# Kernel optimization log

Hardware: AMD Instinct MI355X
Metric: run time of the kernel (lower is better)

The kernel has to match this reference:

```python
import jax, jax.numpy as jnp
import numpy as np

B, T, D = 256, 261, 768      # batch, tokens (1 cls + 4 reg + 16*16 patches), embed_dim
NUM_REG = 4
G = 16                       # patch grid side = 224 // 14
ROI = 3                      # roi_side


def setup_inputs() -> dict:
    key = jax.random.key(0)
    k1, k2 = jax.random.split(key)
    tokens = jax.random.normal(k1, (B, T, D), jnp.float32)
    W_proj = jax.random.normal(k2, (D, D), jnp.float32) * (1.0 / np.sqrt(D))
    b_proj = jnp.zeros((D,), jnp.float32)
    return {"tokens": tokens, "W_proj": W_proj, "b_proj": b_proj}


def _buddy_pool_all(cues, patches2d):
    # cues: [B, C, d]; patches2d: [B, H, W, d]
    Bn, H, W, d = patches2d.shape
    flat = patches2d.reshape(Bn, H * W, d)
    sim = jnp.einsum('bcd,bnd->bcn', cues, flat)          # [B, C, HW]
    idx = jnp.argmax(sim, axis=-1)                         # [B, C]
    h, w = idx // W, idx % W
    r = ROI // 2
    rows = jnp.arange(H)
    cols = jnp.arange(W)
    # clipped ROI window == torch slice(max(0,h-r), min(H,h+r+1)) as a mask
    rmask = (rows[None, None, :] >= (h - r)[..., None]) & (rows[None, None, :] <= (h + r)[..., None])  # [B,C,H]
    cmask = (cols[None, None, :] >= (w - r)[..., None]) & (cols[None, None, :] <= (w + r)[..., None])  # [B,C,W]
    mask = (rmask[..., :, None] & cmask[..., None, :]).astype(patches2d.dtype)  # [B,C,H,W]
    roi_sum = jnp.einsum('bchw,bhwd->bcd', mask, patches2d)
    cnt = jnp.sum(mask, axis=(-2, -1))[..., None]          # 4, 6, or 9 at borders
    return roi_sum / cnt                                   # [B, C, d]


def reference(tokens, W_proj, b_proj):
    t = tokens @ W_proj.T + b_proj                         # nn.Linear projection
    cues = t[:, : 1 + NUM_REG, :]                          # cls + registers: [B,5,d]
    patches2d = t[:, 1 + NUM_REG :, :].reshape(t.shape[0], G, G, D)
    rois = _buddy_pool_all(cues, patches2d)                # [B,5,d]
    toks = jnp.concatenate([cues, rois], axis=1)           # [B,10,d]
    n = jnp.linalg.norm(toks, axis=-1, keepdims=True)
    return toks / jnp.maximum(n, 1e-12)                    # F.normalize
```

## Files before the change

### kernel.cpp

```cpp
#include <hip/hip_runtime.h>
#include <math.h>

constexpr int kB = 256;
constexpr int kT = 261;
constexpr int kD = 768;
constexpr int kC = 5;
constexpr int kG = 16;
constexpr int kP = 256;
constexpr int kTok = kT * kD;
constexpr float kTau = 0.03f;
constexpr int kSlots = 64;

typedef short short8v __attribute__((ext_vector_type(8)));
typedef float f32x4 __attribute__((ext_vector_type(4)));
typedef unsigned short ushort_t;

__device__ inline ushort_t f2bf(float x) {
    unsigned int u = __float_as_uint(x);
    unsigned int r = (u + 0x7FFFu + ((u >> 16) & 1u)) >> 16;
    return (ushort_t)r;
}
__device__ inline float bf2f(ushort_t h) { return __uint_as_float(((unsigned int)h) << 16); }


__global__ __launch_bounds__(256)
void kprep(const float* __restrict__ W,
           ushort_t* __restrict__ Wb_hi, ushort_t* __restrict__ Wb_lo,
           ushort_t* __restrict__ Wt_hi, ushort_t* __restrict__ Wt_lo)
{
    __shared__ ushort_t Lhi[32][36], Llo[32][36];
    const int blk = blockIdx.x, tr = blk / 24, tc = blk % 24;
    const int t = threadIdx.x, r = t >> 3, q = t & 7;
    const int row = tr * 32 + r, col = tc * 32 + q * 4;
    const float4 v = *(const float4*)&W[(size_t)row * kD + col];
    const ushort_t h0 = f2bf(v.x), h1 = f2bf(v.y), h2 = f2bf(v.z), h3 = f2bf(v.w);
    const ushort_t l0 = f2bf(v.x - bf2f(h0)), l1 = f2bf(v.y - bf2f(h1));
    const ushort_t l2 = f2bf(v.z - bf2f(h2)), l3 = f2bf(v.w - bf2f(h3));
    *(ushort4*)&Wb_hi[(size_t)row * kD + col] = make_ushort4(h0, h1, h2, h3);
    *(ushort4*)&Wb_lo[(size_t)row * kD + col] = make_ushort4(l0, l1, l2, l3);
    Lhi[r][q*4+0] = h0; Lhi[r][q*4+1] = h1; Lhi[r][q*4+2] = h2; Lhi[r][q*4+3] = h3;
    Llo[r][q*4+0] = l0; Llo[r][q*4+1] = l1; Llo[r][q*4+2] = l2; Llo[r][q*4+3] = l3;
    __syncthreads();
    const size_t orow = (size_t)(tc * 32 + r) * kD + tr * 32 + q * 4;
    *(ushort4*)&Wt_hi[orow] = make_ushort4(Lhi[q*4+0][r], Lhi[q*4+1][r], Lhi[q*4+2][r], Lhi[q*4+3][r]);
    *(ushort4*)&Wt_lo[orow] = make_ushort4(Llo[q*4+0][r], Llo[q*4+1][r], Llo[q*4+2][r], Llo[q*4+3][r]);
}

template<int MODE>
__global__ __launch_bounds__(256)
void kmm(const float* __restrict__ tokens,
         const ushort_t* __restrict__ Bhi, const ushort_t* __restrict__ Blo,
         const float* __restrict__ bvec, const float* __restrict__ Asrc,
         float* __restrict__ dstA, float* __restrict__ dstB)
{
    __shared__ ushort_t Ah[32][40], Al[32][40];
    __shared__ ushort_t Bh[32][40], Bl[32][40];
    const int mt = blockIdx.x, nt = blockIdx.y, t = threadIdx.x;
    const int w = t >> 6, l = t & 63;
    const int ln = l & 15, kq = l >> 4;
    const int mf = w & 1, nf = w >> 1;
    const int ar = t >> 3, aq = t & 7;
    const int br = t >> 3, bq = t & 7;

    const int am = mt * 32 + ar;
    const float* __restrict__ Ap = (MODE == 0) ? tokens : Asrc;
    const size_t arow = (MODE == 0)
        ? ((size_t)(am / 5) * kTok + (size_t)(am % 5) * kD)
        : ((size_t)am * kD);
    const size_t brow = (size_t)(nt * 32 + br) * kD;

    float4 pa; ushort4 pbh, pbl;
    auto load_regs = [&](int kc) {
        pa  = *(const float4*)&Ap[arow + kc + aq * 4];
        pbh = *(const ushort4*)&Bhi[brow + kc + bq * 4];
        pbl = *(const ushort4*)&Blo[brow + kc + bq * 4];
    };
    auto write_lds = [&]() {
        const ushort_t h0 = f2bf(pa.x), h1 = f2bf(pa.y), h2 = f2bf(pa.z), h3 = f2bf(pa.w);
        const ushort_t a0 = f2bf(pa.x - bf2f(h0)), a1 = f2bf(pa.y - bf2f(h1));
        const ushort_t a2 = f2bf(pa.z - bf2f(h2)), a3 = f2bf(pa.w - bf2f(h3));
        *(ushort4*)&Ah[ar][aq * 4] = make_ushort4(h0, h1, h2, h3);
        *(ushort4*)&Al[ar][aq * 4] = make_ushort4(a0, a1, a2, a3);
        *(ushort4*)&Bh[br][bq * 4] = pbh;
        *(ushort4*)&Bl[br][bq * 4] = pbl;
    };

    f32x4 acc = {0.f, 0.f, 0.f, 0.f};
    auto compute = [&]() {
        const short8v ah  = *(const short8v*)&Ah[mf * 16 + ln][kq * 8];
        const short8v al_ = *(const short8v*)&Al[mf * 16 + ln][kq * 8];
        const short8v bh  = *(const short8v*)&Bh[nf * 16 + ln][kq * 8];
        const short8v bl  = *(const short8v*)&Bl[nf * 16 + ln][kq * 8];
        acc = __builtin_amdgcn_mfma_f32_16x16x32_bf16(al_, bh, acc, 0, 0, 0);
        acc = __builtin_amdgcn_mfma_f32_16x16x32_bf16(ah,  bl, acc, 0, 0, 0);
        acc = __builtin_amdgcn_mfma_f32_16x16x32_bf16(ah,  bh, acc, 0, 0, 0);
    };

    load_regs(0);
    write_lds();
    __syncthreads();
    for (int kc = 32; kc < kD; kc += 32) {
        load_regs(kc);
        compute();
        __syncthreads();
        write_lds();
        __syncthreads();
    }
    compute();

    const int col = nt * 32 + nf * 16 + ln;
    const float bb = (MODE != 1) ? bvec[col] : 0.f;
    #pragma unroll
    for (int r = 0; r < 4; ++r) {
        const int row = mt * 32 + mf * 16 + kq * 4 + r;
        const float val = acc[r] + bb;
        if (MODE == 0) {
            dstA[(size_t)row * kD + col] = val;
            dstB[((size_t)(row / 5) * 10 + (row % 5)) * kD + col] = val;
        } else if (MODE == 1) {
            dstA[(size_t)row * kD + col] = val;
        } else {
            dstA[((size_t)(row / 5) * 10 + 5 + (row % 5)) * kD + col] = val;
        }
    }
}

__global__ __launch_bounds__(256)
void ksim(const float* __restrict__ tokens, const float* __restrict__ u_all,
          float* __restrict__ simsp)
{
    __shared__ ushort_t Uh[6][392], Ul[6][392];
    const int b = blockIdx.x, pq = blockIdx.y, kh = blockIdx.z;
    const int t = threadIdx.x;
    const int w = t >> 6, lane = t & 63;
    const int ln = lane & 15, kq = lane >> 4;
    const size_t tb = (size_t)b * kTok;

    for (int i = t; i < 384; i += 256) {
        const int gd = kh * 384 + i;
        #pragma unroll
        for (int c = 0; c < kC; ++c) {
            const float v = u_all[(size_t)b * kC * kD + (size_t)c * kD + gd];
            const ushort_t h = f2bf(v);
            Uh[c][i] = h; Ul[c][i] = f2bf(v - bf2f(h));
        }
        Uh[kC][i] = 0; Ul[kC][i] = 0;
    }
    __syncthreads();

    const int urow = (ln < kC) ? ln : kC;
    const int n0 = pq * 64 + w * 16;
    const float* __restrict__ prow =
        &tokens[tb + (size_t)(kC + n0 + ln) * kD + kh * 384 + kq * 8];

    f32x4 acc = {0.f, 0.f, 0.f, 0.f};
    #pragma unroll
    for (int c = 0; c < 12; ++c) {
        const float4 fa = *(const float4*)&prow[c * 32];
        const float4 fb = *(const float4*)&prow[c * 32 + 4];
        const float fv[8] = {fa.x, fa.y, fa.z, fa.w, fb.x, fb.y, fb.z, fb.w};
        short8v bh, bl;
        #pragma unroll
        for (int j = 0; j < 8; ++j) {
            const ushort_t h = f2bf(fv[j]);
            bh[j] = (short)h;
            bl[j] = (short)f2bf(fv[j] - bf2f(h));
        }
        const short8v ah  = *(const short8v*)&Uh[urow][c * 32 + kq * 8];
        const short8v al_ = *(const short8v*)&Ul[urow][c * 32 + kq * 8];
        acc = __builtin_amdgcn_mfma_f32_16x16x32_bf16(al_, bh, acc, 0, 0, 0);
        acc = __builtin_amdgcn_mfma_f32_16x16x32_bf16(ah,  bl, acc, 0, 0, 0);
        acc = __builtin_amdgcn_mfma_f32_16x16x32_bf16(ah,  bh, acc, 0, 0, 0);
    }
    float* __restrict__ sp = simsp + (size_t)kh * (1280 * (size_t)kP);
    const int n = n0 + ln;
    if (kq == 0) {
        #pragma unroll
        for (int r = 0; r < 4; ++r)
            sp[((size_t)b * kC + r) * kP + n] = acc[r];
    } else if (kq == 1) {
        sp[((size_t)b * kC + 4) * kP + n] = acc[0];
    }
}

__global__ __launch_bounds__(64)
void ktop(const float* __restrict__ simsp, int* __restrict__ bestn,
          int* __restrict__ cnt, int* __restrict__ flist)
{
    const int pair = blockIdx.x;
    const int lane = threadIdx.x;
    const float* s0 = &simsp[(size_t)pair * kP];
    const float* s1 = &simsp[1280 * (size_t)kP + (size_t)pair * kP];
    float m1 = -3.4e38f, m2 = -3.4e38f; int i1 = 0;
    #pragma unroll
    for (int k = 0; k < 4; ++k) {
        const int n = lane + k * 64;
        const float v = s0[n] + s1[n];
        if (v > m1 || (v == m1 && n < i1)) { m2 = m1; m1 = v; i1 = n; }
        else if (v > m2) m2 = v;
    }
    #pragma unroll
    for (int off = 32; off >= 1; off >>= 1) {
        const float om1 = __shfl_xor(m1, off, 64);
        const int   oi1 = __shfl_xor(i1, off, 64);
        const float om2 = __shfl_xor(m2, off, 64);
        float nm2 = fmaxf(m2, om2);
        if (om1 > m1 || (om1 == m1 && oi1 < i1)) { nm2 = fmaxf(nm2, m1); m1 = om1; i1 = oi1; }
        else nm2 = fmaxf(nm2, om1);
        m2 = nm2;
    }
    if (lane == 0) {
        bestn[pair] = i1;
        if (m1 - m2 < kTau) {
            const int i = atomicAdd(cnt, 1);
            if (i < kSlots) flist[i] = pair;
        }
    }
}

__global__ __launch_bounds__(256)
void kr_tcb(const float* __restrict__ tokens, const float* __restrict__ W,
            const float* __restrict__ bvec, const int* __restrict__ cnt,
            const int* __restrict__ flist, double* __restrict__ tcb64g)
{
    const int slot = blockIdx.x;
    if (slot >= min(*cnt, kSlots)) return;
    const int pair = flist[slot];
    const int b = pair / 5, c = pair % 5;
    const int js = blockIdx.y;
    const int t = threadIdx.x, w = t >> 6, lane = t & 63;
    const size_t tb = (size_t)b * kTok;

    const float* cuep = &tokens[tb + (size_t)c * kD + lane * 4];
    const float4 cf0 = *(const float4*)&cuep[0];
    const float4 cf1 = *(const float4*)&cuep[256];
    const float4 cf2 = *(const float4*)&cuep[512];
    for (int it = 0; it < 16; ++it) {
        const int j = js * 64 + it * 4 + w;
        const float* wr = &W[(size_t)j * kD + lane * 4];
        const float4 w0 = *(const float4*)&wr[0];
        const float4 w1 = *(const float4*)&wr[256];
        const float4 w2 = *(const float4*)&wr[512];
        double acc = (double)w0.x*cf0.x + (double)w0.y*cf0.y + (double)w0.z*cf0.z + (double)w0.w*cf0.w
                   + (double)w1.x*cf1.x + (double)w1.y*cf1.y + (double)w1.z*cf1.z + (double)w1.w*cf1.w
                   + (double)w2.x*cf2.x + (double)w2.y*cf2.y + (double)w2.z*cf2.z + (double)w2.w*cf2.w;
        #pragma unroll
        for (int off = 32; off >= 1; off >>= 1)
            acc += __shfl_xor(acc, off, 64);
        if (lane == 0) tcb64g[(size_t)slot * kD + j] = acc + (double)bvec[j];
    }
}

__global__ __launch_bounds__(256)
void kr_u(const float* __restrict__ W, const int* __restrict__ cnt,
          const double* __restrict__ tcb64g, double* __restrict__ u64g)
{
    const int slot = blockIdx.x;
    if (slot >= min(*cnt, kSlots)) return;
    __shared__ double part[4][64];
    const int t = threadIdx.x;
    const int i = t & 63, jq = t >> 6;
    const int i0 = blockIdx.y * 64;

    const double* tc = &tcb64g[(size_t)slot * kD + jq * 192];
    const float* wp = &W[(size_t)(jq * 192) * kD + i0 + i];
    double acc = 0.0;
    #pragma unroll 8
    for (int j = 0; j < 192; ++j)
        acc += tc[j] * (double)wp[(size_t)j * kD];
    part[jq][i] = acc;
    __syncthreads();
    if (t < 64)
        u64g[(size_t)slot * kD + i0 + t] = part[0][t] + part[1][t] + part[2][t] + part[3][t];
}

__global__ __launch_bounds__(256)
void kr_sim(const float* __restrict__ tokens, const int* __restrict__ cnt,
            const int* __restrict__ flist, const double* __restrict__ u64g,
            double* __restrict__ s64g)
{
    const int slot = blockIdx.x;
    if (slot >= min(*cnt, kSlots)) return;
    __shared__ double u64s[kD];
    const int pair = flist[slot];
    const int b = pair / 5;
    const int ps = blockIdx.y;
    const int t = threadIdx.x, w = t >> 6, lane = t & 63;
    const size_t tb = (size_t)b * kTok;

    u64s[t]       = u64g[(size_t)slot * kD + t];
    u64s[t + 256] = u64g[(size_t)slot * kD + t + 256];
    u64s[t + 512] = u64g[(size_t)slot * kD + t + 512];
    __syncthreads();

    #pragma unroll
    for (int it = 0; it < 8; ++it) {
        const int n = ps * 32 + w * 8 + it;
        const float* p = &tokens[tb + (size_t)(kC + n) * kD + lane * 4];
        const float4 p0 = *(const float4*)&p[0];
        const float4 p1 = *(const float4*)&p[256];
        const float4 p2 = *(const float4*)&p[512];
        const double* ud = &u64s[lane * 4];
        double acc = (double)p0.x*ud[0]   + (double)p0.y*ud[1]   + (double)p0.z*ud[2]   + (double)p0.w*ud[3]
                   + (double)p1.x*ud[256] + (double)p1.y*ud[257] + (double)p1.z*ud[258] + (double)p1.w*ud[259]
                   + (double)p2.x*ud[512] + (double)p2.y*ud[513] + (double)p2.z*ud[514] + (double)p2.w*ud[515];
        #pragma unroll
        for (int off = 32; off >= 1; off >>= 1)
            acc += __shfl_xor(acc, off, 64);
        if (lane == 0) s64g[(size_t)slot * kP + n] = acc;
    }
}

__global__ __launch_bounds__(64)
void kr_arg(const int* __restrict__ cnt, const int* __restrict__ flist,
            const double* __restrict__ s64g, int* __restrict__ bestn)
{
    const int slot = blockIdx.x;
    if (slot >= min(*cnt, kSlots)) return;
    const int lane = threadIdx.x;
    const double* s = &s64g[(size_t)slot * kP];
    double best = -1.0e300; int bi = 0;
    #pragma unroll
    for (int k = 0; k < 4; ++k) {
        const int n = lane + k * 64;
        const double v = s[n];
        if (v > best || (v == best && n < bi)) { best = v; bi = n; }
    }
    #pragma unroll
    for (int off = 32; off >= 1; off >>= 1) {
        const double v2 = __shfl_xor(best, off, 64);
        const int    i2 = __shfl_xor(bi, off, 64);
        if (v2 > best || (v2 == best && i2 < bi)) { best = v2; bi = i2; }
    }
    if (lane == 0) bestn[flist[slot]] = bi;
}

__global__ __launch_bounds__(256)
void kroi(const float* __restrict__ tokens, const int* __restrict__ bestn,
          float* __restrict__ roi)
{
    const int b = blockIdx.x, c = blockIdx.y, t = threadIdx.x;
    const size_t tb = (size_t)b * kTok;
    const int nn = bestn[b * kC + c];
    const int h = nn >> 4, ww = nn & 15;
    const int rlo = max(h - 1, 0), rhi = min(h + 1, kG - 1);
    const int clo = max(ww - 1, 0), chi = min(ww + 1, kG - 1);
    const float inv = 1.0f / (float)((rhi - rlo + 1) * (chi - clo + 1));
    #pragma unroll
    for (int s = 0; s < 3; ++s) {
        const int d = t + s * 256;
        float sum = 0.f;
        for (int rr = rlo; rr <= rhi; ++rr)
            for (int cc = clo; cc <= chi; ++cc)
                sum += tokens[tb + (size_t)(kC + rr * kG + cc) * kD + d];
        roi[((size_t)b * kC + c) * kD + d] = sum * inv;
    }
}

__global__ __launch_bounds__(256)
void knorm(float* __restrict__ out)
{
    __shared__ float wsum[4];
    const int row = blockIdx.x, t = threadIdx.x;
    float* p = out + (size_t)row * kD;
    const float x0 = p[t], x1 = p[t + 256], x2 = p[t + 512];
    float ss = x0 * x0 + x1 * x1 + x2 * x2;
    #pragma unroll
    for (int off = 32; off >= 1; off >>= 1) ss += __shfl_down(ss, off, 64);
    if ((t & 63) == 0) wsum[t >> 6] = ss;
    __syncthreads();
    const float tot = wsum[0] + wsum[1] + wsum[2] + wsum[3];
    const float nrm = fmaxf(sqrtf(tot), 1e-12f);
    p[t] = x0 / nrm; p[t + 256] = x1 / nrm; p[t + 512] = x2 / nrm;
}

extern "C" void kernel_launch(void* const* d_in, const int* in_sizes, int n_in,
                              void* d_out, int out_size, void* d_ws, size_t ws_size,
                              hipStream_t stream) {
    const float* tokens = (const float*)d_in[0];
    const float* W      = (const float*)d_in[1];
    const float* bvec   = (const float*)d_in[2];
    float* out = (float*)d_out;
    float* ws = (float*)d_ws;
    float* simsp = ws;
    float* tcb   = ws;
    float* u_all = ws + 983040;
    float* roi   = ws + 1966080;
    int*   bestn = (int*)(ws + 2949120);
    ushort_t* wsb = (ushort_t*)(ws + 2951680);
    ushort_t* Wb_hi = wsb;
    ushort_t* Wb_lo = wsb + 589824;
    ushort_t* Wt_hi = wsb + 1179648;
    ushort_t* Wt_lo = wsb + 1769472;
    int*    cnt    = (int*)(ws + 4131328);
    int*    flist  = (int*)(ws + 4131329);
    double* tcb64g = (double*)(ws + 4131400);
    double* u64g   = (double*)(ws + 4229704);
    double* s64g   = (double*)(ws + 4328008);

    hipMemsetAsync(cnt, 0, sizeof(int), stream);
    kprep<<<dim3(576), 256, 0, stream>>>(W, Wb_hi, Wb_lo, Wt_hi, Wt_lo);
    kmm<0><<<dim3(40, 24), 256, 0, stream>>>(tokens, Wb_hi, Wb_lo, bvec, nullptr, tcb, out);
    kmm<1><<<dim3(40, 24), 256, 0, stream>>>(tokens, Wt_hi, Wt_lo, bvec, tcb, u_all, nullptr);
    ksim<<<dim3(256, 4, 2), 256, 0, stream>>>(tokens, u_all, simsp);
    ktop<<<dim3(1280), 64, 0, stream>>>(simsp, bestn, cnt, flist);
    kr_tcb<<<dim3(kSlots, 12), 256, 0, stream>>>(tokens, W, bvec, cnt, flist, tcb64g);
    kr_u<<<dim3(kSlots, 12), 256, 0, stream>>>(W, cnt, tcb64g, u64g);
    kr_sim<<<dim3(kSlots, 8), 256, 0, stream>>>(tokens, cnt, flist, u64g, s64g);
    kr_arg<<<dim3(kSlots), 64, 0, stream>>>(cnt, flist, s64g, bestn);
    kroi<<<dim3(256, 5), 256, 0, stream>>>(tokens, bestn, roi);
    kmm<2><<<dim3(40, 24), 256, 0, stream>>>(tokens, Wb_hi, Wb_lo, bvec, roi, out, nullptr);
    knorm<<<dim3(2560), 256, 0, stream>>>(out);
}
```

Baseline: 152.3 us.

## Fuse similarity, top-2 selection and ROI pooling into one per-batch kernel

Result: no change. 150.0 us (median of 2 runs) (-1.5%).

```diff
diff --git a/kernel.cpp b/kernel.cpp
--- a/kernel.cpp
+++ b/kernel.cpp
@@ -26,11 +26,13 @@
 __global__ __launch_bounds__(256)
 void kprep(const float* __restrict__ W,
            ushort_t* __restrict__ Wb_hi, ushort_t* __restrict__ Wb_lo,
-           ushort_t* __restrict__ Wt_hi, ushort_t* __restrict__ Wt_lo)
+           ushort_t* __restrict__ Wt_hi, ushort_t* __restrict__ Wt_lo,
+           int* __restrict__ cnt)
 {
     __shared__ ushort_t Lhi[32][36], Llo[32][36];
     const int blk = blockIdx.x, tr = blk / 24, tc = blk % 24;
     const int t = threadIdx.x, r = t >> 3, q = t & 7;
+    if (blk == 0 && t == 0) *cnt = 0;
     const int row = tr * 32 + r, col = tc * 32 + q * 4;
     const float4 v = *(const float4*)&W[(size_t)row * kD + col];
     const ushort_t h0 = f2bf(v.x), h1 = f2bf(v.y), h2 = f2bf(v.z), h3 = f2bf(v.w);
@@ -125,37 +127,39 @@
     }
 }
 
-__global__ __launch_bounds__(256)
-void ksim(const float* __restrict__ tokens, const float* __restrict__ u_all,
-          float* __restrict__ simsp)
-{
-    __shared__ ushort_t Uh[6][392], Ul[6][392];
-    const int b = blockIdx.x, pq = blockIdx.y, kh = blockIdx.z;
-    const int t = threadIdx.x;
+__global__ __launch_bounds__(1024, 1)
+void ksim_fused(const float* __restrict__ tokens, const float* __restrict__ u_all,
+                int* __restrict__ bestn, int* __restrict__ cnt, int* __restrict__ flist,
+                float* __restrict__ roi)
+{
+    __shared__ ushort_t Uh[6][776], Ul[6][776];
+    __shared__ float simsL[kC][kP];
+    __shared__ int bestnL[kC];
+    __shared__ int flagL;
+    const int b = blockIdx.x, t = threadIdx.x;
     const int w = t >> 6, lane = t & 63;
     const int ln = lane & 15, kq = lane >> 4;
     const size_t tb = (size_t)b * kTok;
-
-    for (int i = t; i < 384; i += 256) {
-        const int gd = kh * 384 + i;
+    if (t == 0) flagL = 0;
+
+    if (t < kD) {
+        const float* ub = u_all + (size_t)b * kC * kD;
         #pragma unroll
         for (int c = 0; c < kC; ++c) {
-            const float v = u_all[(size_t)b * kC * kD + (size_t)c * kD + gd];
+            const float v = ub[(size_t)c * kD + t];
             const ushort_t h = f2bf(v);
-            Uh[c][i] = h; Ul[c][i] = f2bf(v - bf2f(h));
-        }
-        Uh[kC][i] = 0; Ul[kC][i] = 0;
-    }
+            Uh[c][t] = h; Ul[c][t] = f2bf(v - bf2f(h));
+        }
+    }
+    if (t < 776) { Uh[kC][t] = 0; Ul[kC][t] = 0; }
     __syncthreads();
 
     const int urow = (ln < kC) ? ln : kC;
-    const int n0 = pq * 64 + w * 16;
-    const float* __restrict__ prow =
-        &tokens[tb + (size_t)(kC + n0 + ln) * kD + kh * 384 + kq * 8];
-
+    const int n0 = w * 16;
+    const float* __restrict__ prow = &tokens[tb + (size_t)(kC + n0 + ln) * kD + kq * 8];
     f32x4 acc = {0.f, 0.f, 0.f, 0.f};
     #pragma unroll
-    for (int c = 0; c < 12; ++c) {
+    for (int c = 0; c < 24; ++c) {
         const float4 fa = *(const float4*)&prow[c * 32];
         const float4 fb = *(const float4*)&prow[c * 32 + 4];
         const float fv[8] = {fa.x, fa.y, fa.z, fa.w, fb.x, fb.y, fb.z, fb.w};
@@ -172,48 +176,60 @@
         acc = __builtin_amdgcn_mfma_f32_16x16x32_bf16(ah,  bl, acc, 0, 0, 0);
         acc = __builtin_amdgcn_mfma_f32_16x16x32_bf16(ah,  bh, acc, 0, 0, 0);
     }
-    float* __restrict__ sp = simsp + (size_t)kh * (1280 * (size_t)kP);
-    const int n = n0 + ln;
     if (kq == 0) {
         #pragma unroll
-        for (int r = 0; r < 4; ++r)
-            sp[((size_t)b * kC + r) * kP + n] = acc[r];
+        for (int r = 0; r < 4; ++r) simsL[r][n0 + ln] = acc[r];
     } else if (kq == 1) {
-        sp[((size_t)b * kC + 4) * kP + n] = acc[0];
-    }
-}
-
-__global__ __launch_bounds__(64)
-void ktop(const float* __restrict__ simsp, int* __restrict__ bestn,
-          int* __restrict__ cnt, int* __restrict__ flist)
-{
-    const int pair = blockIdx.x;
-    const int lane = threadIdx.x;
-    const float* s0 = &simsp[(size_t)pair * kP];
-    const float* s1 = &simsp[1280 * (size_t)kP + (size_t)pair * kP];
-    float m1 = -3.4e38f, m2 = -3.4e38f; int i1 = 0;
-    #pragma unroll
-    for (int k = 0; k < 4; ++k) {
-        const int n = lane + k * 64;
-        const float v = s0[n] + s1[n];
-        if (v > m1 || (v == m1 && n < i1)) { m2 = m1; m1 = v; i1 = n; }
-        else if (v > m2) m2 = v;
-    }
-    #pragma unroll
-    for (int off = 32; off >= 1; off >>= 1) {
-        const float om1 = __shfl_xor(m1, off, 64);
-        const int   oi1 = __shfl_xor(i1, off, 64);
-        const float om2 = __shfl_xor(m2, off, 64);
-        float nm2 = fmaxf(m2, om2);
-        if (om1 > m1 || (om1 == m1 && oi1 < i1)) { nm2 = fmaxf(nm2, m1); m1 = om1; i1 = oi1; }
-        else nm2 = fmaxf(nm2, om1);
-        m2 = nm2;
-    }
-    if (lane == 0) {
-        bestn[pair] = i1;
-        if (m1 - m2 < kTau) {
-            const int i = atomicAdd(cnt, 1);
-            if (i < kSlots) flist[i] = pair;
+        simsL[4][n0 + ln] = acc[0];
+    }
+    __syncthreads();
+
+    if (w < kC) {
+        const int c = w;
+        float m1 = -3.4e38f, m2 = -3.4e38f; int i1 = 0;
+        #pragma unroll
+        for (int k = 0; k < 4; ++k) {
+            const int n = lane + k * 64;
+            const float v = simsL[c][n];
+            if (v > m1 || (v == m1 && n < i1)) { m2 = m1; m1 = v; i1 = n; }
+            else if (v > m2) m2 = v;
+        }
+        #pragma unroll
+        for (int off = 32; off >= 1; off >>= 1) {
+            const float om1 = __shfl_xor(m1, off, 64);
+            const int   oi1 = __shfl_xor(i1, off, 64);
+            const float om2 = __shfl_xor(m2, off, 64);
+            float nm2 = fmaxf(m2, om2);
+            if (om1 > m1 || (om1 == m1 && oi1 < i1)) { nm2 = fmaxf(nm2, m1); m1 = om1; i1 = oi1; }
+            else nm2 = fmaxf(nm2, om1);
+            m2 = nm2;
+        }
+        if (lane == 0) {
+            bestnL[c] = i1;
+            bestn[b * kC + c] = i1;
+            if (m1 - m2 < kTau) {
+                atomicOr(&flagL, 1 << c);
+                const int i = atomicAdd(cnt, 1);
+                if (i < kSlots) flist[i] = b * kC + c;
+            }
+        }
+    }
+    __syncthreads();
+
+    if (t < kD) {
+        const int d = t;
+        #pragma unroll
+        for (int c = 0; c < kC; ++c) {
+            if (flagL & (1 << c)) continue;
+            const int nn = bestnL[c];
+            const int h = nn >> 4, ww = nn & 15;
+            const int rlo = max(h - 1, 0), rhi = min(h + 1, kG - 1);
+            const int clo = max(ww - 1, 0), chi = min(ww + 1, kG - 1);
+            float sum = 0.f;
+            for (int rr = rlo; rr <= rhi; ++rr)
+                for (int cc = clo; cc <= chi; ++cc)
+                    sum += tokens[tb + (size_t)(kC + rr * kG + cc) * kD + d];
+            roi[((size_t)b * kC + c) * kD + d] = sum / (float)((rhi - rlo + 1) * (chi - clo + 1));
         }
     }
 }
@@ -335,26 +351,26 @@
     if (lane == 0) bestn[flist[slot]] = bi;
 }
 
-__global__ __launch_bounds__(256)
-void kroi(const float* __restrict__ tokens, const int* __restrict__ bestn,
-          float* __restrict__ roi)
-{
-    const int b = blockIdx.x, c = blockIdx.y, t = threadIdx.x;
+__global__ __launch_bounds__(768)
+void kroi_fix(const float* __restrict__ tokens, const int* __restrict__ cnt,
+              const int* __restrict__ flist, const int* __restrict__ bestn,
+              float* __restrict__ roi)
+{
+    const int slot = blockIdx.x;
+    if (slot >= min(*cnt, kSlots)) return;
+    const int pair = flist[slot];
+    const int b = pair / 5, c = pair % 5;
+    const int d = threadIdx.x;
     const size_t tb = (size_t)b * kTok;
-    const int nn = bestn[b * kC + c];
+    const int nn = bestn[pair];
     const int h = nn >> 4, ww = nn & 15;
     const int rlo = max(h - 1, 0), rhi = min(h + 1, kG - 1);
     const int clo = max(ww - 1, 0), chi = min(ww + 1, kG - 1);
-    const float inv = 1.0f / (float)((rhi - rlo + 1) * (chi - clo + 1));
-    #pragma unroll
-    for (int s = 0; s < 3; ++s) {
-        const int d = t + s * 256;
-        float sum = 0.f;
-        for (int rr = rlo; rr <= rhi; ++rr)
-            for (int cc = clo; cc <= chi; ++cc)
-                sum += tokens[tb + (size_t)(kC + rr * kG + cc) * kD + d];
-        roi[((size_t)b * kC + c) * kD + d] = sum * inv;
-    }
+    float sum = 0.f;
+    for (int rr = rlo; rr <= rhi; ++rr)
+        for (int cc = clo; cc <= chi; ++cc)
+            sum += tokens[tb + (size_t)(kC + rr * kG + cc) * kD + d];
+    roi[((size_t)b * kC + c) * kD + d] = sum / (float)((rhi - rlo + 1) * (chi - clo + 1));
 }
 
 __global__ __launch_bounds__(256)
@@ -382,7 +398,6 @@
     const float* bvec   = (const float*)d_in[2];
     float* out = (float*)d_out;
     float* ws = (float*)d_ws;
-    float* simsp = ws;
     float* tcb   = ws;
     float* u_all = ws + 983040;
     float* roi   = ws + 1966080;
@@ -398,17 +413,15 @@
     double* u64g   = (double*)(ws + 4229704);
     double* s64g   = (double*)(ws + 4328008);
 
-    hipMemsetAsync(cnt, 0, sizeof(int), stream);
-    kprep<<<dim3(576), 256, 0, stream>>>(W, Wb_hi, Wb_lo, Wt_hi, Wt_lo);
+    kprep<<<dim3(576), 256, 0, stream>>>(W, Wb_hi, Wb_lo, Wt_hi, Wt_lo, cnt);
     kmm<0><<<dim3(40, 24), 256, 0, stream>>>(tokens, Wb_hi, Wb_lo, bvec, nullptr, tcb, out);
     kmm<1><<<dim3(40, 24), 256, 0, stream>>>(tokens, Wt_hi, Wt_lo, bvec, tcb, u_all, nullptr);
-    ksim<<<dim3(256, 4, 2), 256, 0, stream>>>(tokens, u_all, simsp);
-    ktop<<<dim3(1280), 64, 0, stream>>>(simsp, bestn, cnt, flist);
+    ksim_fused<<<dim3(256), 1024, 0, stream>>>(tokens, u_all, bestn, cnt, flist, roi);
     kr_tcb<<<dim3(kSlots, 12), 256, 0, stream>>>(tokens, W, bvec, cnt, flist, tcb64g);
     kr_u<<<dim3(kSlots, 12), 256, 0, stream>>>(W, cnt, tcb64g, u64g);
     kr_sim<<<dim3(kSlots, 8), 256, 0, stream>>>(tokens, cnt, flist, u64g, s64g);
     kr_arg<<<dim3(kSlots), 64, 0, stream>>>(cnt, flist, s64g, bestn);
-    kroi<<<dim3(256, 5), 256, 0, stream>>>(tokens, bestn, roi);
+    kroi_fix<<<dim3(kSlots), 768, 0, stream>>>(tokens, cnt, flist, bestn, roi);
     kmm<2><<<dim3(40, 24), 256, 0, stream>>>(tokens, Wb_hi, Wb_lo, bvec, roi, out, nullptr);
     knorm<<<dim3(2560), 256, 0, stream>>>(out);
 }
```
